# Kernel optimization log

Hardware: AMD Instinct MI355X
Metric: run time of the kernel (lower is better)

## Reference

```python
import jax, jax.numpy as jnp
import numpy as np

B, S, E = 32, 128, 128
NQ, NS = 100000, 512
QN, SN = 4, 10
S_MAX = 4
NEG = -1e30


def setup_inputs() -> dict:
    key = jax.random.key(0)
    ks = jax.random.split(key, 24)
    def nrm(k, shape, sc):
        return jax.random.normal(k, shape, jnp.float32) * sc
    inp = {}
    inp['question'] = jax.random.randint(ks[0], (B, S), 0, NQ, jnp.int32)
    inp['response'] = jax.random.randint(ks[1], (B, S), 0, 2, jnp.int32)
    inp['mask'] = jax.random.randint(ks[2], (B, S), 0, 2, jnp.int32)
    inp['q_neighbors'] = jax.random.randint(ks[3], (NQ, QN), 0, NS, jnp.int32)
    inp['s_neighbors'] = jax.random.randint(ks[4], (NS, SN), 0, NQ, jnp.int32)
    sidx = jax.random.randint(ks[5], (NQ, S_MAX), 0, NS, jnp.int32)
    inp['qs_table'] = jnp.zeros((NQ, NS), jnp.float32).at[jnp.arange(NQ)[:, None], sidx].set(1.0)
    inp['emb_q'] = nrm(ks[6], (NQ, E), 1.0)
    inp['emb_s'] = nrm(ks[7], (NS, E), 1.0)
    inp['emb_r'] = nrm(ks[8], (2, E), 1.0)
    s_in = 1.0 / np.sqrt(2 * E).astype(np.float32)
    s_e = 1.0 / np.sqrt(E).astype(np.float32)
    inp['W_ih'] = nrm(ks[9], (4 * E, 2 * E), s_in)
    inp['b_ih'] = nrm(ks[10], (4 * E,), s_in)
    inp['b_hh'] = nrm(ks[11], (4 * E,), s_in)
    inp['W_agg'] = nrm(ks[12], (3, E, E), s_e)
    inp['b_agg'] = nrm(ks[13], (3, E), s_e)
    inp['W_last'] = nrm(ks[14], (E, E), s_e)
    inp['b_last'] = nrm(ks[15], (E,), s_e)
    inp['W_query'] = nrm(ks[16], (E, E), s_e)
    inp['b_query'] = nrm(ks[17], (E,), s_e)
    inp['W_key'] = nrm(ks[18], (E, E), s_e)
    inp['b_key'] = nrm(ks[19], (E,), s_e)
    inp['w_W'] = nrm(ks[20], (2 * E,), s_in)
    inp['b_W'] = nrm(ks[21], (), s_in)
    return inp


def _forward(question, response, mask, q_neighbors, s_neighbors, qs_table,
             emb_q, emb_s, emb_r, W_ih, b_ih, b_hh, W_agg, b_agg, W_last, b_last,
             W_query, b_query, W_key, b_key, w_W, b_W):
    Bq, Sq = question.shape
    Ed = emb_q.shape[1]
    AGG = W_agg.shape[0]
    w_q, w_k = w_W[:Ed], w_W[Ed:]
    c_pad = jnp.tanh(b_query) @ w_k  # attention logit piece of an all-zero padded state
    pos = jnp.arange(Sq)

    def step(state_history, xs):
        t, q_t, r_t, m_t, q_next = xs
        # ---- multi-hop neighbor gather (q -> s -> q -> s) ----
        n1 = q_neighbors[q_t]              # [B,QN] skill ids
        n2 = s_neighbors[n1]               # [B,QN,SN] question ids
        n3 = q_neighbors[n2]               # [B,QN,SN,QN] skill ids
        e = [emb_q[q_t], emb_s[n1], emb_q[n2], emb_s[n3]]
        # triangular mean-aggregate (dropout is identity in eval mode)
        for i in range(AGG):
            for j in range(AGG - i):
                e[j] = jnp.tanh((e[j + 1].mean(-2) + e[j]) @ W_agg[j].T + b_agg[j])
        agg = jnp.tanh(e[0] @ W_last.T + b_last)
        emb_qt = jnp.where((m_t == 1)[:, None], agg, emb_q[q_t])
        # ---- LSTMCell with zero initial (h, c): W_hh @ 0 drops out, b_hh remains ----
        x = jnp.concatenate([emb_qt, emb_r[r_t]], -1)
        gates = x @ W_ih.T + b_ih + b_hh
        gi, gf, gg, go = jnp.split(gates, 4, -1)
        h = jax.nn.sigmoid(go) * jnp.tanh(jax.nn.sigmoid(gi) * jnp.tanh(gg))
        # ---- skills related to next question; zero-padded rows contribute exactly 0 ----
        vals, sidx = jax.lax.top_k(qs_table[q_next], S_MAX)
        emb_sk = emb_s[sidx] * (vals > 0.0)[..., None]
        qs_concat = jnp.concatenate([emb_q[q_next][:, None], emb_sk], 1)  # [B,1+S_MAX,E]
        # ---- hard recap: history steps whose question is a 2-hop neighbor of q_next ----
        q_rel = s_neighbors[q_neighbors[q_next]].reshape(Bq, -1)          # [B,QN*SN]
        matches = (question[:, :, None] == q_rel[:, None, :]).any(-1) & (pos[None, :] < t)
        n_sel = matches.sum(-1)
        P = (jnp.max(n_sel) - n_sel).astype(jnp.float32)  # zero-pad count to per-batch max
        # ---- predict: MLP_W(concat(Q,K)) is rank-1 => logit = a[b,q] + c[b,s] ----
        a = jnp.tanh(qs_concat @ W_key.T + b_key) @ w_q + b_W             # [B,Qd]
        c_hist = jnp.tanh(state_history @ W_query.T + b_query) @ w_k      # [B,S]
        c_cur = jnp.tanh(h @ W_query.T + b_query) @ w_k                   # [B]
        lh = jnp.where(matches[:, None, :], a[:, :, None] + c_hist[:, None, :], NEG)
        lc = a + c_cur[:, None]
        lp = a + c_pad
        m = jnp.maximum(jnp.maximum(lh.max(-1), lc), lp)
        Eh = jnp.exp(lh - m[:, :, None])
        Ec = jnp.exp(lc - m)
        Ep = jnp.exp(lp - m)
        g_hist = jnp.einsum('bqe,bse->bqs', qs_concat, state_history)
        g_cur = jnp.einsum('bqe,be->bq', qs_concat, h)
        denom = Eh.sum(-1) + Ec + P[:, None] * Ep  # zero-pad states counted analytically
        num = (Eh * g_hist).sum(-1) + Ec * g_cur   # pads multiply g=0 -> no numerator term
        y = jax.nn.sigmoid(jnp.sum(num / denom, axis=1))
        # original skips the state write at t == 0 (slot 0 stays zero forever)
        state_history = state_history.at[:, t].set(jnp.where(t > 0, h, jnp.zeros_like(h)))
        return state_history, y

    ts = jnp.arange(Sq - 1)
    xs = (ts, question[:, :-1].T, response[:, :-1].T, mask[:, :-1].T, question[:, 1:].T)
    init = jnp.zeros((Bq, Sq, Ed), jnp.float32)
    _, ys = jax.lax.scan(step, init, xs)
    return jnp.zeros((Bq, Sq), jnp.float32).at[:, 0].set(0.5).at[:, 1:].set(ys.T)


def reference(question, response, mask, q_neighbors, s_neighbors, qs_table,
              emb_q, emb_s, emb_r, W_ih, b_ih, b_hh, W_agg, b_agg, W_last, b_last,
              W_query, b_query, W_key, b_key, w_W, b_W):
    return _forward(question, response, mask, q_neighbors, s_neighbors, qs_table,
                    emb_q, emb_s, emb_r, W_ih, b_ih, b_hh, W_agg, b_agg, W_last, b_last,
                    W_query, b_query, W_key, b_key, w_W, b_W)
```

## Files before the change

kernel.cpp:

```cpp
#include <hip/hip_runtime.h>
#include <stdint.h>

#define NB 32
#define SEQ 128
#define EMB 128
#define NSTEP 127
#define NS 512

__device__ __forceinline__ float ftanh(float x){ float e=__expf(2.f*x); return 1.f-2.f/(e+1.f); }
__device__ __forceinline__ float fsig(float x){ return 1.f/(1.f+__expf(-x)); }
__device__ __forceinline__ float4 ld4(const float* p){ return *(const float4*)p; }

#define FMA4(acc, xv, a0, a1, a2, a3) \
  acc.x = fmaf(xv.x, a0.x, fmaf(xv.y, a1.x, fmaf(xv.z, a2.x, fmaf(xv.w, a3.x, acc.x)))); \
  acc.y = fmaf(xv.x, a0.y, fmaf(xv.y, a1.y, fmaf(xv.z, a2.y, fmaf(xv.w, a3.y, acc.y)))); \
  acc.z = fmaf(xv.x, a0.z, fmaf(xv.y, a1.z, fmaf(xv.z, a2.z, fmaf(xv.w, a3.z, acc.z)))); \
  acc.w = fmaf(xv.x, a0.w, fmaf(xv.y, a1.w, fmaf(xv.z, a2.w, fmaf(xv.w, a3.w, acc.w))));

template<int K, int XS>
__device__ __forceinline__ void gemm8(const float* __restrict__ WT, int NEtot,
                                      const float* __restrict__ Xl,
                                      const float* __restrict__ bias,
                                      float* __restrict__ outb )
{
  const int tid = threadIdx.x;
  const int et = tid & 31;
  const int rt = tid >> 5;
  const float* wp = WT + et*4;
  const float* xr = Xl + rt*XS;
  constexpr int G = K/4;
  float4 acc = {0.f,0.f,0.f,0.f};
  float4 w0 = ld4(wp);
  float4 w1 = ld4(wp + NEtot);
  float4 w2 = ld4(wp + 2*NEtot);
  float4 w3 = ld4(wp + 3*NEtot);
  const float* wq = wp + (size_t)4*NEtot;
  float4 m0 = ld4(wq);
  float4 m1 = ld4(wq + NEtot);
  float4 m2 = ld4(wq + 2*NEtot);
  float4 m3 = ld4(wq + 3*NEtot);
  #pragma unroll 2
  for (int g = 0; g + 2 < G; g += 2) {
    const float* wa = wp + (size_t)(4*(g+2))*NEtot;
    float4 n0 = ld4(wa);
    float4 n1 = ld4(wa + NEtot);
    float4 n2 = ld4(wa + 2*NEtot);
    float4 n3 = ld4(wa + 3*NEtot);
    float4 xa = ld4(xr + 4*g);
    FMA4(acc, xa, w0, w1, w2, w3);
    w0=n0; w1=n1; w2=n2; w3=n3;
    const float* wb = wp + (size_t)(4*(g+3))*NEtot;
    float4 o0 = ld4(wb);
    float4 o1 = ld4(wb + NEtot);
    float4 o2 = ld4(wb + 2*NEtot);
    float4 o3 = ld4(wb + 3*NEtot);
    float4 xb = ld4(xr + 4*(g+1));
    FMA4(acc, xb, m0, m1, m2, m3);
    m0=o0; m1=o1; m2=o2; m3=o3;
  }
  {
    float4 xa = ld4(xr + 4*(G-2));
    FMA4(acc, xa, w0, w1, w2, w3);
    float4 xb = ld4(xr + 4*(G-1));
    FMA4(acc, xb, m0, m1, m2, m3);
  }
  float4 bb = ld4(bias + et*4);
  acc.x+=bb.x; acc.y+=bb.y; acc.z+=bb.z; acc.w+=bb.w;
  *(float4*)(outb + rt*132 + et*4) = acc;
}

__global__ __launch_bounds__(256) void k_T(
    const float* __restrict__ W_agg, const float* __restrict__ W_last,
    const float* __restrict__ W_query, const float* __restrict__ W_ih,
    const float* __restrict__ b_ih, const float* __restrict__ b_hh,
    const float* __restrict__ b_query, const float* __restrict__ w_W,
    float* __restrict__ WT012, float* __restrict__ WLT, float* __restrict__ WQT,
    float* __restrict__ WIHT, float* __restrict__ BIH, float* __restrict__ CPAD,
    float* __restrict__ G1, int* __restrict__ Pmaxi)
{
  const int gid = blockIdx.x*256 + threadIdx.x;
  const int gsz = gridDim.x*256;
  for (int i = gid; i < 49152; i += gsz) {
    int j = i >> 14, rem = i & 16383, k = rem >> 7, e = rem & 127;
    WT012[i] = W_agg[j*16384 + e*128 + k];
  }
  for (int i = gid; i < 16384; i += gsz) {
    int k = i >> 7, e = i & 127;
    WLT[i] = W_last[e*128 + k];
    WQT[i] = W_query[e*128 + k];
  }
  for (int i = gid; i < 131072; i += gsz) {
    int k = i >> 9, e = i & 511;
    WIHT[i] = W_ih[e*256 + k];
  }
  for (int i = gid; i < 65536; i += gsz) G1[i] = 0.f;
  for (int i = gid; i < 512; i += gsz) BIH[i] = b_ih[i] + b_hh[i];
  for (int i = gid; i < 128; i += gsz) Pmaxi[i] = 0;
  if (blockIdx.x == 0) {
    __shared__ float red[256];
    float v = (threadIdx.x < 128) ? ftanh(b_query[threadIdx.x]) * w_W[128 + threadIdx.x] : 0.f;
    red[threadIdx.x] = v; __syncthreads();
    #pragma unroll
    for (int s = 128; s > 0; s >>= 1) {
      if (threadIdx.x < s) red[threadIdx.x] += red[threadIdx.x + s];
      __syncthreads();
    }
    if (threadIdx.x == 0) CPAD[0] = red[0];
  }
}

__global__ __launch_bounds__(256) void k_pre(
    const int* __restrict__ s_neighbors, const int* __restrict__ q_neighbors,
    const float* __restrict__ emb_q, const float* __restrict__ emb_s,
    const float* __restrict__ WT012, const float* __restrict__ b_agg,
    float* __restrict__ E1, float* __restrict__ G1)
{
  __shared__ float XA[8*132];
  __shared__ float XB[8*132];
  __shared__ int idx[80];
  __shared__ int n3[32];
  const int tid = threadIdx.x;
  const int blk = blockIdx.x;
  if (blk < 64) {
    const int s0 = blk*8;
    if (tid < 80) idx[tid] = s_neighbors[s0*10 + tid];
    __syncthreads();
    {
      int r = tid >> 5, e4 = (tid & 31) << 2;
      float4 a = ld4(emb_s + (size_t)(s0+r)*128 + e4);
      float sx=0,sy=0,sz=0,sw=0;
      #pragma unroll
      for (int jj = 0; jj < 10; ++jj) {
        float4 q = ld4(emb_q + (size_t)idx[r*10+jj]*128 + e4);
        sx+=q.x; sy+=q.y; sz+=q.z; sw+=q.w;
      }
      float4 o; o.x=a.x+0.1f*sx; o.y=a.y+0.1f*sy; o.z=a.z+0.1f*sz; o.w=a.w+0.1f*sw;
      *(float4*)(XA + r*132 + e4) = o;
    }
    __syncthreads();
    gemm8<128,132>(WT012 + 16384, 128, XA, b_agg + 128, XB);
    __syncthreads();
    for (int f = tid; f < 1024; f += 256) {
      int r = f >> 7, e = f & 127;
      E1[(size_t)(s0+r)*128 + e] = ftanh(XB[r*132 + e]);
    }
  } else {
    const int p0 = (blk-64)*8;
    if (tid < 8) idx[tid] = s_neighbors[p0 + tid];
    __syncthreads();
    if (tid < 32) n3[tid] = q_neighbors[(size_t)idx[tid>>2]*4 + (tid&3)];
    __syncthreads();
    {
      int r = tid >> 5, e4 = (tid & 31) << 2;
      float4 a = ld4(emb_q + (size_t)idx[r]*128 + e4);
      float sx=0,sy=0,sz=0,sw=0;
      #pragma unroll
      for (int k = 0; k < 4; ++k) {
        float4 q = ld4(emb_s + (size_t)n3[r*4+k]*128 + e4);
        sx+=q.x; sy+=q.y; sz+=q.z; sw+=q.w;
      }
      float4 o; o.x=a.x+0.25f*sx; o.y=a.y+0.25f*sy; o.z=a.z+0.25f*sz; o.w=a.w+0.25f*sw;
      *(float4*)(XA + r*132 + e4) = o;
    }
    __syncthreads();
    gemm8<128,132>(WT012 + 32768, 128, XA, b_agg + 256, XB);
    __syncthreads();
    for (int f = tid; f < 1024; f += 256) {
      int r = f >> 7, e = f & 127;
      atomicAdd(&G1[(size_t)((p0+r)/10)*128 + e], ftanh(XB[r*132 + e]));
    }
  }
}

__global__ __launch_bounds__(256) void k_pre2(
    const float* __restrict__ E1, const float* __restrict__ G1,
    const float* __restrict__ WT012, const float* __restrict__ b_agg,
    float* __restrict__ E2)
{
  __shared__ float XA[8*132];
  __shared__ float XB[8*132];
  const int tid = threadIdx.x;
  const int s0 = blockIdx.x*8;
  for (int f = tid; f < 1024; f += 256) {
    int r = f >> 7, e = f & 127;
    XA[r*132 + e] = 0.1f*G1[(size_t)(s0+r)*128 + e] + E1[(size_t)(s0+r)*128 + e];
  }
  __syncthreads();
  gemm8<128,132>(WT012 + 16384, 128, XA, b_agg + 128, XB);
  __syncthreads();
  for (int f = tid; f < 1024; f += 256) {
    int r = f >> 7, e = f & 127;
    E2[(size_t)(s0+r)*128 + e] = ftanh(XB[r*132 + e]);
  }
}

__global__ __launch_bounds__(256) void k_chain(
    const int* __restrict__ question, const int* __restrict__ response,
    const int* __restrict__ maskp, const int* __restrict__ q_neighbors,
    const float* __restrict__ emb_q, const float* __restrict__ emb_s,
    const float* __restrict__ emb_r,
    const float* __restrict__ WT012, const float* __restrict__ WLT,
    const float* __restrict__ WQT, const float* __restrict__ WIHT,
    const float* __restrict__ BIH,
    const float* __restrict__ b_agg, const float* __restrict__ b_last,
    const float* __restrict__ b_query, const float* __restrict__ w_W,
    const float* __restrict__ E1, const float* __restrict__ E2,
    float* __restrict__ Hfull, float* __restrict__ Cq)
{
  __shared__ float XA[8*132];
  __shared__ float XB[8*132];
  __shared__ float M1[8*132];
  __shared__ float M2[8*132];
  __shared__ float XC[8*264];
  __shared__ int qts[8], rts[8], mts[8], n1s[32];

  const int tid = threadIdx.x;
  const int blk = blockIdx.x;

  if (tid < 8) {
    int rid = blk*8 + tid;
    int b = rid / 127, t = rid - b*127;
    qts[tid] = question[b*SEQ + t];
    rts[tid] = response[b*SEQ + t];
    mts[tid] = maskp[b*SEQ + t];
  }
  __syncthreads();
  if (tid < 32) n1s[tid] = q_neighbors[(size_t)qts[tid>>2]*4 + (tid&3)];
  __syncthreads();
  {
    int r = tid >> 5, e4 = (tid & 31) << 2;
    const int* nn = n1s + r*4;
    float4 a = ld4(emb_q + (size_t)qts[r]*128 + e4);
    float s1x=0,s1y=0,s1z=0,s1w=0, s2x=0,s2y=0,s2z=0,s2w=0, s3x=0,s3y=0,s3z=0,s3w=0;
    #pragma unroll
    for (int i = 0; i < 4; ++i) {
      float4 q1 = ld4(emb_s + (size_t)nn[i]*128 + e4);
      float4 q2 = ld4(E1 + (size_t)nn[i]*128 + e4);
      float4 q3 = ld4(E2 + (size_t)nn[i]*128 + e4);
      s1x+=q1.x; s1y+=q1.y; s1z+=q1.z; s1w+=q1.w;
      s2x+=q2.x; s2y+=q2.y; s2z+=q2.z; s2w+=q2.w;
      s3x+=q3.x; s3y+=q3.y; s3z+=q3.z; s3w+=q3.w;
    }
    float4 o; o.x=a.x+0.25f*s1x; o.y=a.y+0.25f*s1y; o.z=a.z+0.25f*s1z; o.w=a.w+0.25f*s1w;
    *(float4*)(XA + r*132 + e4) = o;
    float4 p; p.x=0.25f*s2x; p.y=0.25f*s2y; p.z=0.25f*s2z; p.w=0.25f*s2w;
    *(float4*)(M1 + r*132 + e4) = p;
    float4 u; u.x=0.25f*s3x; u.y=0.25f*s3y; u.z=0.25f*s3z; u.w=0.25f*s3w;
    *(float4*)(M2 + r*132 + e4) = u;
  }
  __syncthreads();
  gemm8<128,132>(WT012, 128, XA, b_agg, XB);
  __syncthreads();
  for (int f = tid; f < 1056; f += 256) XB[f] = M1[f] + ftanh(XB[f]);
  __syncthreads();
  gemm8<128,132>(WT012, 128, XB, b_agg, XA);
  __syncthreads();
  for (int f = tid; f < 1056; f += 256) XA[f] = M2[f] + ftanh(XA[f]);
  __syncthreads();
  gemm8<128,132>(WT012, 128, XA, b_agg, XB);
  __syncthreads();
  for (int f = tid; f < 1056; f += 256) XB[f] = ftanh(XB[f]);
  __syncthreads();
  gemm8<128,132>(WLT, 128, XB, b_last, XA);
  __syncthreads();
  for (int f = tid; f < 1024; f += 256) {
    int r = f >> 7, e = f & 127;
    float agg = ftanh(XA[r*132 + e]);
    XC[r*264 + e] = (mts[r] == 1) ? agg : emb_q[(size_t)qts[r]*128 + e];
    XC[r*264 + 128 + e] = emb_r[rts[r]*128 + e];
  }
  __syncthreads();
  gemm8<256,264>(WIHT,       512, XC, BIH,       XA);
  gemm8<256,264>(WIHT + 256, 512, XC, BIH + 256, XB);
  gemm8<256,264>(WIHT + 384, 512, XC, BIH + 384, M1);
  __syncthreads();
  for (int f = tid; f < 1024; f += 256) {
    int r = f >> 7, e = f & 127;
    float gi = XA[r*132 + e], gg = XB[r*132 + e], go = M1[r*132 + e];
    float h = fsig(go) * ftanh(fsig(gi) * ftanh(gg));
    XC[r*264 + e] = h;
    Hfull[(size_t)(blk*8 + r)*128 + e] = h;
  }
  __syncthreads();
  gemm8<128,264>(WQT, 128, XC, b_query, XA);
  __syncthreads();
  {
    const int et = tid & 31, rt = tid >> 5;
    float4 o = ld4(XA + rt*132 + et*4);
    float4 wv = ld4(w_W + 128 + et*4);
    float s = ftanh(o.x)*wv.x + ftanh(o.y)*wv.y + ftanh(o.z)*wv.z + ftanh(o.w)*wv.w;
    #pragma unroll
    for (int off = 16; off > 0; off >>= 1) s += __shfl_down(s, off);
    if (et == 0) Cq[blk*8 + rt] = s;
  }
}

__global__ __launch_bounds__(64) void k_match(
    const int* __restrict__ question, const int* __restrict__ q_neighbors,
    const int* __restrict__ s_neighbors,
    int* __restrict__ nsel, unsigned long long* __restrict__ mwords,
    int* __restrict__ Pmaxi)
{
  __shared__ int qr[40];
  const int tid = threadIdx.x;
  const int t = blockIdx.x;
  const int b = blockIdx.y;
  const int q_next = question[b*SEQ + t + 1];
  if (tid < 40)
    qr[tid] = s_neighbors[(size_t)q_neighbors[(size_t)q_next*4 + tid/10]*10 + tid%10];
  __syncthreads();
  int q0 = question[b*SEQ + tid];
  int q1 = question[b*SEQ + 64 + tid];
  bool p0 = false, p1 = false;
  #pragma unroll 8
  for (int i = 0; i < 40; ++i) { p0 |= (q0 == qr[i]); p1 |= (q1 == qr[i]); }
  p0 &= (tid < t);
  p1 &= (64 + tid < t);
  unsigned long long w0 = __ballot(p0);
  unsigned long long w1 = __ballot(p1);
  if (tid == 0) {
    mwords[((size_t)b*NSTEP + t)*2 + 0] = w0;
    mwords[((size_t)b*NSTEP + t)*2 + 1] = w1;
    int ns = __popcll(w0) + __popcll(w1);
    nsel[b*NSTEP + t] = ns;
    atomicMax(&Pmaxi[t], ns);
  }
}

__device__ __forceinline__ float wredsum(float v) {
  #pragma unroll
  for (int o = 32; o > 0; o >>= 1) v += __shfl_down(v, o);
  return v;
}
__device__ __forceinline__ float wredmax(float v) {
  #pragma unroll
  for (int o = 32; o > 0; o >>= 1) v = fmaxf(v, __shfl_down(v, o));
  return v;
}

__global__ __launch_bounds__(128) void k_attn(
    const int* __restrict__ question, const float* __restrict__ qs_table,
    const float* __restrict__ emb_q, const float* __restrict__ emb_s,
    const float* __restrict__ CPAD,
    const float* __restrict__ Hfull, const float* __restrict__ Cq,
    const int* __restrict__ nsel, const unsigned long long* __restrict__ mwords,
    const int* __restrict__ Pmaxi, float* __restrict__ out)
{
  __shared__ float us[128];
  __shared__ int cols[8];
  __shared__ int cnt;
  __shared__ float smx[2];
  __shared__ float s3[2][3];
  const int tid = threadIdx.x;
  const int wid = tid >> 6;
  const int bid = blockIdx.x;
  const int b = bid / NSTEP, t = bid % NSTEP;
  const size_t bt = (size_t)b*NSTEP + t;
  const int q_next = question[b*SEQ + t + 1];

  if (tid == 0) cnt = 0;
  __syncthreads();
  {
    float4 v = ld4(qs_table + (size_t)q_next*NS + tid*4);
    if (v.x > 0.f) { int p = atomicAdd(&cnt, 1); if (p < 8) cols[p] = tid*4; }
    if (v.y > 0.f) { int p = atomicAdd(&cnt, 1); if (p < 8) cols[p] = tid*4+1; }
    if (v.z > 0.f) { int p = atomicAdd(&cnt, 1); if (p < 8) cols[p] = tid*4+2; }
    if (v.w > 0.f) { int p = atomicAdd(&cnt, 1); if (p < 8) cols[p] = tid*4+3; }
  }
  __syncthreads();
  const int nc = min(cnt, 4);
  {
    float ue = emb_q[(size_t)q_next*EMB + tid];
    for (int i = 0; i < nc; ++i) ue += emb_s[(size_t)cols[i]*EMB + tid];
    us[tid] = ue;
  }
  const float c_pad = CPAD[0];
  const float P = (float)(Pmaxi[t] - nsel[bt]);

  const unsigned long long w0 = mwords[bt*2 + 0];
  const unsigned long long w1 = mwords[bt*2 + 1];
  const bool matched = (tid < 64) ? ((w0 >> tid) & 1ull)
                                  : ((w1 >> (tid - 64)) & 1ull);
  const float c_cur = Cq[bt];
  float Cp = matched ? ((tid == 0) ? c_pad : Cq[(size_t)b*NSTEP + tid]) : -3.0e38f;
  float mh = wredmax(Cp);
  if ((tid & 63) == 0) smx[wid] = mh;
  __syncthreads();
  float M = fmaxf(fmaxf(smx[0], smx[1]), fmaxf(c_cur, c_pad));
  float wgt = matched ? __expf(Cp - M) : 0.f;
  float dotp = 0.f;
  if (matched && tid >= 1) {
    const float* hp = Hfull + ((size_t)b*NSTEP + tid)*EMB;
    float s = 0.f;
    #pragma unroll 8
    for (int e = 0; e < 128; e += 4) {
      float4 h4 = ld4(hp + e);
      s = fmaf(us[e],h4.x, fmaf(us[e+1],h4.y, fmaf(us[e+2],h4.z, fmaf(us[e+3],h4.w, s))));
    }
    dotp = s;
  }
  float gcp = us[tid] * Hfull[bt*EMB + tid];
  float a0 = wredsum(wgt);
  float a1 = wredsum(wgt * dotp);
  float a2 = wredsum(gcp);
  if ((tid & 63) == 0) { s3[wid][0] = a0; s3[wid][1] = a1; s3[wid][2] = a2; }
  __syncthreads();
  if (tid == 0) {
    float Sexp = s3[0][0] + s3[1][0];
    float Snum = s3[0][1] + s3[1][1];
    float gc   = s3[0][2] + s3[1][2];
    float Ec = __expf(c_cur - M), Ep = __expf(c_pad - M);
    float D = Sexp + Ec + P * Ep;
    float numt = Snum + Ec * gc;
    out[b*SEQ + t + 1] = fsig(numt / D);
    if (t == 0) out[b*SEQ] = 0.5f;
  }
}

extern "C" void kernel_launch(void* const* d_in, const int* in_sizes, int n_in,
                              void* d_out, int out_size, void* d_ws, size_t ws_size,
                              hipStream_t stream) {
  const int* question    = (const int*)d_in[0];
  const int* response    = (const int*)d_in[1];
  const int* maskp       = (const int*)d_in[2];
  const int* q_neighbors = (const int*)d_in[3];
  const int* s_neighbors = (const int*)d_in[4];
  const float* qs_table  = (const float*)d_in[5];
  const float* emb_q     = (const float*)d_in[6];
  const float* emb_s     = (const float*)d_in[7];
  const float* emb_r     = (const float*)d_in[8];
  const float* W_ih      = (const float*)d_in[9];
  const float* b_ih      = (const float*)d_in[10];
  const float* b_hh      = (const float*)d_in[11];
  const float* W_agg     = (const float*)d_in[12];
  const float* b_agg     = (const float*)d_in[13];
  const float* W_last    = (const float*)d_in[14];
  const float* b_last    = (const float*)d_in[15];
  const float* W_query   = (const float*)d_in[16];
  const float* b_query   = (const float*)d_in[17];
  const float* w_W       = (const float*)d_in[20];
  float* out = (float*)d_out;

  float* ws = (float*)d_ws;
  float* WT012 = ws;
  float* WLT   = ws + 49152;
  float* WQT   = ws + 65536;
  float* WIHT  = ws + 81920;
  float* BIH   = ws + 212992;
  float* CPAD  = ws + 213504;
  float* E1    = ws + 213520;
  float* G1    = ws + 279056;
  float* E2    = ws + 344592;
  float* Hfull = ws + 410128;
  float* Cq    = ws + 930320;
  int*   Pmaxi = (int*)(ws + 934384);
  int*   nselp = (int*)(ws + 934512);
  unsigned long long* mwords =
      (unsigned long long*)(((uintptr_t)(ws + 938576) + 15) & ~(uintptr_t)15);

  k_T<<<dim3(64), dim3(256), 0, stream>>>(
      W_agg, W_last, W_query, W_ih, b_ih, b_hh, b_query, w_W,
      WT012, WLT, WQT, WIHT, BIH, CPAD, G1, Pmaxi);
  k_pre<<<dim3(704), dim3(256), 0, stream>>>(
      s_neighbors, q_neighbors, emb_q, emb_s, WT012, b_agg, E1, G1);
  k_pre2<<<dim3(64), dim3(256), 0, stream>>>(E1, G1, WT012, b_agg, E2);
  k_chain<<<dim3(508), dim3(256), 0, stream>>>(
      question, response, maskp, q_neighbors, emb_q, emb_s, emb_r,
      WT012, WLT, WQT, WIHT, BIH, b_agg, b_last, b_query, w_W,
      E1, E2, Hfull, Cq);
  k_match<<<dim3(NSTEP, NB), dim3(64), 0, stream>>>(
      question, q_neighbors, s_neighbors, nselp, mwords, Pmaxi);
  k_attn<<<dim3(NB*NSTEP), dim3(128), 0, stream>>>(
      question, qs_table, emb_q, emb_s, CPAD, Hfull, Cq,
      nselp, mwords, Pmaxi, out);
}
```

Measured before the change: 430.1 us.

## Fuse all stages into one persistent kernel with grid-wide atomic barriers

Replaces the six separate launches (transpose, two precompute passes, chain, match, attention) with one persistent 512-block kernel that runs each stage in turn, separated by software grid barriers built on agent-scope atomics and a spin-wait. The match work is folded into the transpose phase and the attention work is batched two units per block. The aim is to remove per-launch overhead and inter-kernel idle gaps. In exchange it relies on all 512 blocks being co-resident (launch_bounds 256,2), otherwise the barriers deadlock, and it adds spin-wait and barrier latency between stages.

After: 701.0 us. +63.0%, slower.

```diff
diff --git a/kernel.cpp b/kernel.cpp
--- a/kernel.cpp
+++ b/kernel.cpp
@@ -6,6 +6,8 @@
 #define EMB 128
 #define NSTEP 127
 #define NS 512
+#define NBLK 512
+#define NUNIT 4064
 
 __device__ __forceinline__ float ftanh(float x){ float e=__expf(2.f*x); return 1.f-2.f/(e+1.f); }
 __device__ __forceinline__ float fsig(float x){ return 1.f/(1.f+__expf(-x)); }
@@ -19,9 +21,8 @@
 
 template<int K, int XS>
 __device__ __forceinline__ void gemm8(const float* __restrict__ WT, int NEtot,
-                                      const float* __restrict__ Xl,
-                                      const float* __restrict__ bias,
-                                      float* __restrict__ outb )
+                                      const float* Xl, const float* __restrict__ bias,
+                                      float* outb )
 {
   const int tid = threadIdx.x;
   const int et = tid & 31;
@@ -69,264 +70,6 @@
   *(float4*)(outb + rt*132 + et*4) = acc;
 }
 
-__global__ __launch_bounds__(256) void k_T(
-    const float* __restrict__ W_agg, const float* __restrict__ W_last,
-    const float* __restrict__ W_query, const float* __restrict__ W_ih,
-    const float* __restrict__ b_ih, const float* __restrict__ b_hh,
-    const float* __restrict__ b_query, const float* __restrict__ w_W,
-    float* __restrict__ WT012, float* __restrict__ WLT, float* __restrict__ WQT,
-    float* __restrict__ WIHT, float* __restrict__ BIH, float* __restrict__ CPAD,
-    float* __restrict__ G1, int* __restrict__ Pmaxi)
-{
-  const int gid = blockIdx.x*256 + threadIdx.x;
-  const int gsz = gridDim.x*256;
-  for (int i = gid; i < 49152; i += gsz) {
-    int j = i >> 14, rem = i & 16383, k = rem >> 7, e = rem & 127;
-    WT012[i] = W_agg[j*16384 + e*128 + k];
-  }
-  for (int i = gid; i < 16384; i += gsz) {
-    int k = i >> 7, e = i & 127;
-    WLT[i] = W_last[e*128 + k];
-    WQT[i] = W_query[e*128 + k];
-  }
-  for (int i = gid; i < 131072; i += gsz) {
-    int k = i >> 9, e = i & 511;
-    WIHT[i] = W_ih[e*256 + k];
-  }
-  for (int i = gid; i < 65536; i += gsz) G1[i] = 0.f;
-  for (int i = gid; i < 512; i += gsz) BIH[i] = b_ih[i] + b_hh[i];
-  for (int i = gid; i < 128; i += gsz) Pmaxi[i] = 0;
-  if (blockIdx.x == 0) {
-    __shared__ float red[256];
-    float v = (threadIdx.x < 128) ? ftanh(b_query[threadIdx.x]) * w_W[128 + threadIdx.x] : 0.f;
-    red[threadIdx.x] = v; __syncthreads();
-    #pragma unroll
-    for (int s = 128; s > 0; s >>= 1) {
-      if (threadIdx.x < s) red[threadIdx.x] += red[threadIdx.x + s];
-      __syncthreads();
-    }
-    if (threadIdx.x == 0) CPAD[0] = red[0];
-  }
-}
-
-__global__ __launch_bounds__(256) void k_pre(
-    const int* __restrict__ s_neighbors, const int* __restrict__ q_neighbors,
-    const float* __restrict__ emb_q, const float* __restrict__ emb_s,
-    const float* __restrict__ WT012, const float* __restrict__ b_agg,
-    float* __restrict__ E1, float* __restrict__ G1)
-{
-  __shared__ float XA[8*132];
-  __shared__ float XB[8*132];
-  __shared__ int idx[80];
-  __shared__ int n3[32];
-  const int tid = threadIdx.x;
-  const int blk = blockIdx.x;
-  if (blk < 64) {
-    const int s0 = blk*8;
-    if (tid < 80) idx[tid] = s_neighbors[s0*10 + tid];
-    __syncthreads();
-    {
-      int r = tid >> 5, e4 = (tid & 31) << 2;
-      float4 a = ld4(emb_s + (size_t)(s0+r)*128 + e4);
-      float sx=0,sy=0,sz=0,sw=0;
-      #pragma unroll
-      for (int jj = 0; jj < 10; ++jj) {
-        float4 q = ld4(emb_q + (size_t)idx[r*10+jj]*128 + e4);
-        sx+=q.x; sy+=q.y; sz+=q.z; sw+=q.w;
-      }
-      float4 o; o.x=a.x+0.1f*sx; o.y=a.y+0.1f*sy; o.z=a.z+0.1f*sz; o.w=a.w+0.1f*sw;
-      *(float4*)(XA + r*132 + e4) = o;
-    }
-    __syncthreads();
-    gemm8<128,132>(WT012 + 16384, 128, XA, b_agg + 128, XB);
-    __syncthreads();
-    for (int f = tid; f < 1024; f += 256) {
-      int r = f >> 7, e = f & 127;
-      E1[(size_t)(s0+r)*128 + e] = ftanh(XB[r*132 + e]);
-    }
-  } else {
-    const int p0 = (blk-64)*8;
-    if (tid < 8) idx[tid] = s_neighbors[p0 + tid];
-    __syncthreads();
-    if (tid < 32) n3[tid] = q_neighbors[(size_t)idx[tid>>2]*4 + (tid&3)];
-    __syncthreads();
-    {
-      int r = tid >> 5, e4 = (tid & 31) << 2;
-      float4 a = ld4(emb_q + (size_t)idx[r]*128 + e4);
-      float sx=0,sy=0,sz=0,sw=0;
-      #pragma unroll
-      for (int k = 0; k < 4; ++k) {
-        float4 q = ld4(emb_s + (size_t)n3[r*4+k]*128 + e4);
-        sx+=q.x; sy+=q.y; sz+=q.z; sw+=q.w;
-      }
-      float4 o; o.x=a.x+0.25f*sx; o.y=a.y+0.25f*sy; o.z=a.z+0.25f*sz; o.w=a.w+0.25f*sw;
-      *(float4*)(XA + r*132 + e4) = o;
-    }
-    __syncthreads();
-    gemm8<128,132>(WT012 + 32768, 128, XA, b_agg + 256, XB);
-    __syncthreads();
-    for (int f = tid; f < 1024; f += 256) {
-      int r = f >> 7, e = f & 127;
-      atomicAdd(&G1[(size_t)((p0+r)/10)*128 + e], ftanh(XB[r*132 + e]));
-    }
-  }
-}
-
-__global__ __launch_bounds__(256) void k_pre2(
-    const float* __restrict__ E1, const float* __restrict__ G1,
-    const float* __restrict__ WT012, const float* __restrict__ b_agg,
-    float* __restrict__ E2)
-{
-  __shared__ float XA[8*132];
-  __shared__ float XB[8*132];
-  const int tid = threadIdx.x;
-  const int s0 = blockIdx.x*8;
-  for (int f = tid; f < 1024; f += 256) {
-    int r = f >> 7, e = f & 127;
-    XA[r*132 + e] = 0.1f*G1[(size_t)(s0+r)*128 + e] + E1[(size_t)(s0+r)*128 + e];
-  }
-  __syncthreads();
-  gemm8<128,132>(WT012 + 16384, 128, XA, b_agg + 128, XB);
-  __syncthreads();
-  for (int f = tid; f < 1024; f += 256) {
-    int r = f >> 7, e = f & 127;
-    E2[(size_t)(s0+r)*128 + e] = ftanh(XB[r*132 + e]);
-  }
-}
-
-__global__ __launch_bounds__(256) void k_chain(
-    const int* __restrict__ question, const int* __restrict__ response,
-    const int* __restrict__ maskp, const int* __restrict__ q_neighbors,
-    const float* __restrict__ emb_q, const float* __restrict__ emb_s,
-    const float* __restrict__ emb_r,
-    const float* __restrict__ WT012, const float* __restrict__ WLT,
-    const float* __restrict__ WQT, const float* __restrict__ WIHT,
-    const float* __restrict__ BIH,
-    const float* __restrict__ b_agg, const float* __restrict__ b_last,
-    const float* __restrict__ b_query, const float* __restrict__ w_W,
-    const float* __restrict__ E1, const float* __restrict__ E2,
-    float* __restrict__ Hfull, float* __restrict__ Cq)
-{
-  __shared__ float XA[8*132];
-  __shared__ float XB[8*132];
-  __shared__ float M1[8*132];
-  __shared__ float M2[8*132];
-  __shared__ float XC[8*264];
-  __shared__ int qts[8], rts[8], mts[8], n1s[32];
-
-  const int tid = threadIdx.x;
-  const int blk = blockIdx.x;
-
-  if (tid < 8) {
-    int rid = blk*8 + tid;
-    int b = rid / 127, t = rid - b*127;
-    qts[tid] = question[b*SEQ + t];
-    rts[tid] = response[b*SEQ + t];
-    mts[tid] = maskp[b*SEQ + t];
-  }
-  __syncthreads();
-  if (tid < 32) n1s[tid] = q_neighbors[(size_t)qts[tid>>2]*4 + (tid&3)];
-  __syncthreads();
-  {
-    int r = tid >> 5, e4 = (tid & 31) << 2;
-    const int* nn = n1s + r*4;
-    float4 a = ld4(emb_q + (size_t)qts[r]*128 + e4);
-    float s1x=0,s1y=0,s1z=0,s1w=0, s2x=0,s2y=0,s2z=0,s2w=0, s3x=0,s3y=0,s3z=0,s3w=0;
-    #pragma unroll
-    for (int i = 0; i < 4; ++i) {
-      float4 q1 = ld4(emb_s + (size_t)nn[i]*128 + e4);
-      float4 q2 = ld4(E1 + (size_t)nn[i]*128 + e4);
-      float4 q3 = ld4(E2 + (size_t)nn[i]*128 + e4);
-      s1x+=q1.x; s1y+=q1.y; s1z+=q1.z; s1w+=q1.w;
-      s2x+=q2.x; s2y+=q2.y; s2z+=q2.z; s2w+=q2.w;
-      s3x+=q3.x; s3y+=q3.y; s3z+=q3.z; s3w+=q3.w;
-    }
-    float4 o; o.x=a.x+0.25f*s1x; o.y=a.y+0.25f*s1y; o.z=a.z+0.25f*s1z; o.w=a.w+0.25f*s1w;
-    *(float4*)(XA + r*132 + e4) = o;
-    float4 p; p.x=0.25f*s2x; p.y=0.25f*s2y; p.z=0.25f*s2z; p.w=0.25f*s2w;
-    *(float4*)(M1 + r*132 + e4) = p;
-    float4 u; u.x=0.25f*s3x; u.y=0.25f*s3y; u.z=0.25f*s3z; u.w=0.25f*s3w;
-    *(float4*)(M2 + r*132 + e4) = u;
-  }
-  __syncthreads();
-  gemm8<128,132>(WT012, 128, XA, b_agg, XB);
-  __syncthreads();
-  for (int f = tid; f < 1056; f += 256) XB[f] = M1[f] + ftanh(XB[f]);
-  __syncthreads();
-  gemm8<128,132>(WT012, 128, XB, b_agg, XA);
-  __syncthreads();
-  for (int f = tid; f < 1056; f += 256) XA[f] = M2[f] + ftanh(XA[f]);
-  __syncthreads();
-  gemm8<128,132>(WT012, 128, XA, b_agg, XB);
-  __syncthreads();
-  for (int f = tid; f < 1056; f += 256) XB[f] = ftanh(XB[f]);
-  __syncthreads();
-  gemm8<128,132>(WLT, 128, XB, b_last, XA);
-  __syncthreads();
-  for (int f = tid; f < 1024; f += 256) {
-    int r = f >> 7, e = f & 127;
-    float agg = ftanh(XA[r*132 + e]);
-    XC[r*264 + e] = (mts[r] == 1) ? agg : emb_q[(size_t)qts[r]*128 + e];
-    XC[r*264 + 128 + e] = emb_r[rts[r]*128 + e];
-  }
-  __syncthreads();
-  gemm8<256,264>(WIHT,       512, XC, BIH,       XA);
-  gemm8<256,264>(WIHT + 256, 512, XC, BIH + 256, XB);
-  gemm8<256,264>(WIHT + 384, 512, XC, BIH + 384, M1);
-  __syncthreads();
-  for (int f = tid; f < 1024; f += 256) {
-    int r = f >> 7, e = f & 127;
-    float gi = XA[r*132 + e], gg = XB[r*132 + e], go = M1[r*132 + e];
-    float h = fsig(go) * ftanh(fsig(gi) * ftanh(gg));
-    XC[r*264 + e] = h;
-    Hfull[(size_t)(blk*8 + r)*128 + e] = h;
-  }
-  __syncthreads();
-  gemm8<128,264>(WQT, 128, XC, b_query, XA);
-  __syncthreads();
-  {
-    const int et = tid & 31, rt = tid >> 5;
-    float4 o = ld4(XA + rt*132 + et*4);
-    float4 wv = ld4(w_W + 128 + et*4);
-    float s = ftanh(o.x)*wv.x + ftanh(o.y)*wv.y + ftanh(o.z)*wv.z + ftanh(o.w)*wv.w;
-    #pragma unroll
-    for (int off = 16; off > 0; off >>= 1) s += __shfl_down(s, off);
-    if (et == 0) Cq[blk*8 + rt] = s;
-  }
-}
-
-__global__ __launch_bounds__(64) void k_match(
-    const int* __restrict__ question, const int* __restrict__ q_neighbors,
-    const int* __restrict__ s_neighbors,
-    int* __restrict__ nsel, unsigned long long* __restrict__ mwords,
-    int* __restrict__ Pmaxi)
-{
-  __shared__ int qr[40];
-  const int tid = threadIdx.x;
-  const int t = blockIdx.x;
-  const int b = blockIdx.y;
-  const int q_next = question[b*SEQ + t + 1];
-  if (tid < 40)
-    qr[tid] = s_neighbors[(size_t)q_neighbors[(size_t)q_next*4 + tid/10]*10 + tid%10];
-  __syncthreads();
-  int q0 = question[b*SEQ + tid];
-  int q1 = question[b*SEQ + 64 + tid];
-  bool p0 = false, p1 = false;
-  #pragma unroll 8
-  for (int i = 0; i < 40; ++i) { p0 |= (q0 == qr[i]); p1 |= (q1 == qr[i]); }
-  p0 &= (tid < t);
-  p1 &= (64 + tid < t);
-  unsigned long long w0 = __ballot(p0);
-  unsigned long long w1 = __ballot(p1);
-  if (tid == 0) {
-    mwords[((size_t)b*NSTEP + t)*2 + 0] = w0;
-    mwords[((size_t)b*NSTEP + t)*2 + 1] = w1;
-    int ns = __popcll(w0) + __popcll(w1);
-    nsel[b*NSTEP + t] = ns;
-    atomicMax(&Pmaxi[t], ns);
-  }
-}
-
 __device__ __forceinline__ float wredsum(float v) {
   #pragma unroll
   for (int o = 32; o > 0; o >>= 1) v += __shfl_down(v, o);
@@ -338,82 +81,351 @@
   return v;
 }
 
-__global__ __launch_bounds__(128) void k_attn(
-    const int* __restrict__ question, const float* __restrict__ qs_table,
+__device__ __forceinline__ void gsync(int* bar, int idx, int nb) {
+  __syncthreads();
+  if (threadIdx.x == 0) {
+    __threadfence();
+    int prev = __hip_atomic_fetch_add(&bar[idx*32], 1, __ATOMIC_ACQ_REL,
+                                      __HIP_MEMORY_SCOPE_AGENT);
+    if (prev == nb - 1) {
+      __hip_atomic_store(&bar[idx*32 + 16], 1, __ATOMIC_RELEASE,
+                         __HIP_MEMORY_SCOPE_AGENT);
+    } else {
+      while (__hip_atomic_load(&bar[idx*32 + 16], __ATOMIC_ACQUIRE,
+                               __HIP_MEMORY_SCOPE_AGENT) == 0)
+        __builtin_amdgcn_s_sleep(8);
+    }
+    __threadfence();
+  }
+  __syncthreads();
+}
+
+__global__ void k_zero(int* __restrict__ bar, int* __restrict__ Pmaxi) {
+  int i = threadIdx.x;
+  if (i < 128) bar[i] = 0;
+  if (i < 128) Pmaxi[i] = 0;
+}
+
+__global__ __launch_bounds__(256, 2) void k_fused(
+    const int* __restrict__ question, const int* __restrict__ response,
+    const int* __restrict__ maskp, const int* __restrict__ q_neighbors,
+    const int* __restrict__ s_neighbors, const float* __restrict__ qs_table,
     const float* __restrict__ emb_q, const float* __restrict__ emb_s,
-    const float* __restrict__ CPAD,
-    const float* __restrict__ Hfull, const float* __restrict__ Cq,
-    const int* __restrict__ nsel, const unsigned long long* __restrict__ mwords,
-    const int* __restrict__ Pmaxi, float* __restrict__ out)
+    const float* __restrict__ emb_r,
+    const float* __restrict__ W_ih, const float* __restrict__ b_ih,
+    const float* __restrict__ b_hh, const float* __restrict__ W_agg,
+    const float* __restrict__ b_agg, const float* __restrict__ W_last,
+    const float* __restrict__ b_last, const float* __restrict__ W_query,
+    const float* __restrict__ b_query, const float* __restrict__ w_W,
+    float* __restrict__ WT012, float* __restrict__ WLT, float* __restrict__ WQT,
+    float* __restrict__ WIHT, float* __restrict__ BIH, float* __restrict__ CPAD,
+    float* __restrict__ E1, float* __restrict__ G1, float* __restrict__ E2,
+    float* __restrict__ Hfull, float* __restrict__ Cq,
+    int* __restrict__ Pmaxi, int* __restrict__ nsel,
+    unsigned long long* __restrict__ mwords, int* __restrict__ bar,
+    float* __restrict__ out)
 {
-  __shared__ float us[128];
-  __shared__ int cols[8];
-  __shared__ int cnt;
-  __shared__ float smx[2];
-  __shared__ float s3[2][3];
+  __shared__ float pool[6336];
+  __shared__ int ipool[256];
+  __shared__ unsigned long long wvw[4];
+  float* XA = pool;
+  float* XB = pool + 1056;
+  float* M1 = pool + 2112;
+  float* M2 = pool + 3168;
+  float* XC = pool + 4224;
+
   const int tid = threadIdx.x;
-  const int wid = tid >> 6;
-  const int bid = blockIdx.x;
-  const int b = bid / NSTEP, t = bid % NSTEP;
-  const size_t bt = (size_t)b*NSTEP + t;
-  const int q_next = question[b*SEQ + t + 1];
-
-  if (tid == 0) cnt = 0;
-  __syncthreads();
+  const int blk = blockIdx.x;
+
   {
-    float4 v = ld4(qs_table + (size_t)q_next*NS + tid*4);
-    if (v.x > 0.f) { int p = atomicAdd(&cnt, 1); if (p < 8) cols[p] = tid*4; }
-    if (v.y > 0.f) { int p = atomicAdd(&cnt, 1); if (p < 8) cols[p] = tid*4+1; }
-    if (v.z > 0.f) { int p = atomicAdd(&cnt, 1); if (p < 8) cols[p] = tid*4+2; }
-    if (v.w > 0.f) { int p = atomicAdd(&cnt, 1); if (p < 8) cols[p] = tid*4+3; }
-  }
-  __syncthreads();
-  const int nc = min(cnt, 4);
+    const int gid = blk*256 + tid;
+    const int gsz = NBLK*256;
+    for (int i = gid; i < 49152; i += gsz) {
+      int j = i >> 14, rem = i & 16383, k = rem >> 7, e = rem & 127;
+      WT012[i] = W_agg[j*16384 + e*128 + k];
+    }
+    for (int i = gid; i < 16384; i += gsz) {
+      int k = i >> 7, e = i & 127;
+      WLT[i] = W_last[e*128 + k];
+      WQT[i] = W_query[e*128 + k];
+    }
+    for (int i = gid; i < 131072; i += gsz) {
+      int k = i >> 9, e = i & 511;
+      WIHT[i] = W_ih[e*256 + k];
+    }
+    for (int i = gid; i < 65536; i += gsz) G1[i] = 0.f;
+    if (gid < 512) BIH[gid] = b_ih[gid] + b_hh[gid];
+    if (blk == 0) {
+      float v = (tid < 128) ? ftanh(b_query[tid]) * w_W[128 + tid] : 0.f;
+      pool[tid] = v; __syncthreads();
+      #pragma unroll
+      for (int s = 128; s > 0; s >>= 1) {
+        if (tid < s) pool[tid] += pool[tid + s];
+        __syncthreads();
+      }
+      if (tid == 0) CPAD[0] = pool[0];
+      __syncthreads();
+    }
+    const int half = tid >> 7, lt = tid & 127;
+    for (int it = 0; it < 4; ++it) {
+      int u = blk*8 + it*2 + half;
+      if (u >= NUNIT) u = NUNIT - 1;
+      int b = u / NSTEP, t = u - b*NSTEP;
+      const int q_next = question[b*SEQ + t + 1];
+      int* qr = ipool + half*40;
+      if (lt < 40)
+        qr[lt] = s_neighbors[(size_t)q_neighbors[(size_t)q_next*4 + lt/10]*10 + lt%10];
+      __syncthreads();
+      int qp = question[b*SEQ + lt];
+      bool p = false;
+      #pragma unroll 8
+      for (int i = 0; i < 40; ++i) p |= (qp == qr[i]);
+      p &= (lt < t);
+      unsigned long long bal = __ballot(p);
+      if ((tid & 63) == 0) {
+        mwords[((size_t)b*NSTEP + t)*2 + ((tid >> 6) & 1)] = bal;
+        wvw[tid >> 6] = bal;
+      }
+      __syncthreads();
+      if (lt == 0) {
+        unsigned long long a0 = wvw[half*2], a1 = wvw[half*2 + 1];
+        int ns = __popcll(a0) + __popcll(a1);
+        nsel[b*NSTEP + t] = ns;
+        atomicMax(&Pmaxi[t], ns);
+      }
+      __syncthreads();
+    }
+  }
+  gsync(bar, 0, NBLK);
+
+  for (int u = blk; u < 704; u += NBLK) {
+    int* idx = ipool;
+    int* n3i = ipool + 80;
+    if (u < 64) {
+      const int s0 = u*8;
+      if (tid < 80) idx[tid] = s_neighbors[s0*10 + tid];
+      __syncthreads();
+      {
+        int r = tid >> 5, e4 = (tid & 31) << 2;
+        float4 a = ld4(emb_s + (size_t)(s0+r)*128 + e4);
+        float sx=0,sy=0,sz=0,sw=0;
+        #pragma unroll
+        for (int jj = 0; jj < 10; ++jj) {
+          float4 q = ld4(emb_q + (size_t)idx[r*10+jj]*128 + e4);
+          sx+=q.x; sy+=q.y; sz+=q.z; sw+=q.w;
+        }
+        float4 o; o.x=a.x+0.1f*sx; o.y=a.y+0.1f*sy; o.z=a.z+0.1f*sz; o.w=a.w+0.1f*sw;
+        *(float4*)(XA + r*132 + e4) = o;
+      }
+      __syncthreads();
+      gemm8<128,132>(WT012 + 16384, 128, XA, b_agg + 128, XB);
+      __syncthreads();
+      for (int f = tid; f < 1024; f += 256) {
+        int r = f >> 7, e = f & 127;
+        E1[(size_t)(s0+r)*128 + e] = ftanh(XB[r*132 + e]);
+      }
+    } else {
+      const int p0 = (u-64)*8;
+      if (tid < 8) idx[tid] = s_neighbors[p0 + tid];
+      __syncthreads();
+      if (tid < 32) n3i[tid] = q_neighbors[(size_t)idx[tid>>2]*4 + (tid&3)];
+      __syncthreads();
+      {
+        int r = tid >> 5, e4 = (tid & 31) << 2;
+        float4 a = ld4(emb_q + (size_t)idx[r]*128 + e4);
+        float sx=0,sy=0,sz=0,sw=0;
+        #pragma unroll
+        for (int k = 0; k < 4; ++k) {
+          float4 q = ld4(emb_s + (size_t)n3i[r*4+k]*128 + e4);
+          sx+=q.x; sy+=q.y; sz+=q.z; sw+=q.w;
+        }
+        float4 o; o.x=a.x+0.25f*sx; o.y=a.y+0.25f*sy; o.z=a.z+0.25f*sz; o.w=a.w+0.25f*sw;
+        *(float4*)(XA + r*132 + e4) = o;
+      }
+      __syncthreads();
+      gemm8<128,132>(WT012 + 32768, 128, XA, b_agg + 256, XB);
+      __syncthreads();
+      for (int f = tid; f < 1024; f += 256) {
+        int r = f >> 7, e = f & 127;
+        atomicAdd(&G1[(size_t)((p0+r)/10)*128 + e], ftanh(XB[r*132 + e]));
+      }
+    }
+    __syncthreads();
+  }
+  gsync(bar, 1, NBLK);
+
+  if (blk < 64) {
+    const int s0 = blk*8;
+    for (int f = tid; f < 1024; f += 256) {
+      int r = f >> 7, e = f & 127;
+      XA[r*132 + e] = 0.1f*G1[(size_t)(s0+r)*128 + e] + E1[(size_t)(s0+r)*128 + e];
+    }
+    __syncthreads();
+    gemm8<128,132>(WT012 + 16384, 128, XA, b_agg + 128, XB);
+    __syncthreads();
+    for (int f = tid; f < 1024; f += 256) {
+      int r = f >> 7, e = f & 127;
+      E2[(size_t)(s0+r)*128 + e] = ftanh(XB[r*132 + e]);
+    }
+  }
+  gsync(bar, 2, NBLK);
+
+  if (blk < 508) {
+    int* qts = ipool;
+    int* rts = ipool + 8;
+    int* mts = ipool + 16;
+    int* n1s = ipool + 24;
+    if (tid < 8) {
+      int rid = blk*8 + tid;
+      int b = rid / 127, t = rid - b*127;
+      qts[tid] = question[b*SEQ + t];
+      rts[tid] = response[b*SEQ + t];
+      mts[tid] = maskp[b*SEQ + t];
+    }
+    __syncthreads();
+    if (tid < 32) n1s[tid] = q_neighbors[(size_t)qts[tid>>2]*4 + (tid&3)];
+    __syncthreads();
+    {
+      int r = tid >> 5, e4 = (tid & 31) << 2;
+      const int* nn = n1s + r*4;
+      float4 a = ld4(emb_q + (size_t)qts[r]*128 + e4);
+      float s1x=0,s1y=0,s1z=0,s1w=0, s2x=0,s2y=0,s2z=0,s2w=0, s3x=0,s3y=0,s3z=0,s3w=0;
+      #pragma unroll
+      for (int i = 0; i < 4; ++i) {
+        float4 q1 = ld4(emb_s + (size_t)nn[i]*128 + e4);
+        float4 q2 = ld4(E1 + (size_t)nn[i]*128 + e4);
+        float4 q3 = ld4(E2 + (size_t)nn[i]*128 + e4);
+        s1x+=q1.x; s1y+=q1.y; s1z+=q1.z; s1w+=q1.w;
+        s2x+=q2.x; s2y+=q2.y; s2z+=q2.z; s2w+=q2.w;
+        s3x+=q3.x; s3y+=q3.y; s3z+=q3.z; s3w+=q3.w;
+      }
+      float4 o; o.x=a.x+0.25f*s1x; o.y=a.y+0.25f*s1y; o.z=a.z+0.25f*s1z; o.w=a.w+0.25f*s1w;
+      *(float4*)(XA + r*132 + e4) = o;
+      float4 p; p.x=0.25f*s2x; p.y=0.25f*s2y; p.z=0.25f*s2z; p.w=0.25f*s2w;
+      *(float4*)(M1 + r*132 + e4) = p;
+      float4 u; u.x=0.25f*s3x; u.y=0.25f*s3y; u.z=0.25f*s3z; u.w=0.25f*s3w;
+      *(float4*)(M2 + r*132 + e4) = u;
+    }
+    __syncthreads();
+    gemm8<128,132>(WT012, 128, XA, b_agg, XB);
+    __syncthreads();
+    for (int f = tid; f < 1056; f += 256) XB[f] = M1[f] + ftanh(XB[f]);
+    __syncthreads();
+    gemm8<128,132>(WT012, 128, XB, b_agg, XA);
+    __syncthreads();
+    for (int f = tid; f < 1056; f += 256) XA[f] = M2[f] + ftanh(XA[f]);
+    __syncthreads();
+    gemm8<128,132>(WT012, 128, XA, b_agg, XB);
+    __syncthreads();
+    for (int f = tid; f < 1056; f += 256) XB[f] = ftanh(XB[f]);
+    __syncthreads();
+    gemm8<128,132>(WLT, 128, XB, b_last, XA);
+    __syncthreads();
+    for (int f = tid; f < 1024; f += 256) {
+      int r = f >> 7, e = f & 127;
+      float agg = ftanh(XA[r*132 + e]);
+      XC[r*264 + e] = (mts[r] == 1) ? agg : emb_q[(size_t)qts[r]*128 + e];
+      XC[r*264 + 128 + e] = emb_r[rts[r]*128 + e];
+    }
+    __syncthreads();
+    gemm8<256,264>(WIHT,       512, XC, BIH,       XA);
+    gemm8<256,264>(WIHT + 256, 512, XC, BIH + 256, XB);
+    gemm8<256,264>(WIHT + 384, 512, XC, BIH + 384, M1);
+    __syncthreads();
+    for (int f = tid; f < 1024; f += 256) {
+      int r = f >> 7, e = f & 127;
+      float gi = XA[r*132 + e], gg = XB[r*132 + e], go = M1[r*132 + e];
+      float h = fsig(go) * ftanh(fsig(gi) * ftanh(gg));
+      XC[r*264 + e] = h;
+      Hfull[(size_t)(blk*8 + r)*128 + e] = h;
+    }
+    __syncthreads();
+    gemm8<128,264>(WQT, 128, XC, b_query, XA);
+    __syncthreads();
+    {
+      const int et = tid & 31, rt = tid >> 5;
+      float4 o = ld4(XA + rt*132 + et*4);
+      float4 wv = ld4(w_W + 128 + et*4);
+      float s = ftanh(o.x)*wv.x + ftanh(o.y)*wv.y + ftanh(o.z)*wv.z + ftanh(o.w)*wv.w;
+      #pragma unroll
+      for (int off = 16; off > 0; off >>= 1) s += __shfl_down(s, off);
+      if (et == 0) Cq[blk*8 + rt] = s;
+    }
+  }
+  gsync(bar, 3, NBLK);
+
   {
-    float ue = emb_q[(size_t)q_next*EMB + tid];
-    for (int i = 0; i < nc; ++i) ue += emb_s[(size_t)cols[i]*EMB + tid];
-    us[tid] = ue;
-  }
-  const float c_pad = CPAD[0];
-  const float P = (float)(Pmaxi[t] - nsel[bt]);
-
-  const unsigned long long w0 = mwords[bt*2 + 0];
-  const unsigned long long w1 = mwords[bt*2 + 1];
-  const bool matched = (tid < 64) ? ((w0 >> tid) & 1ull)
-                                  : ((w1 >> (tid - 64)) & 1ull);
-  const float c_cur = Cq[bt];
-  float Cp = matched ? ((tid == 0) ? c_pad : Cq[(size_t)b*NSTEP + tid]) : -3.0e38f;
-  float mh = wredmax(Cp);
-  if ((tid & 63) == 0) smx[wid] = mh;
-  __syncthreads();
-  float M = fmaxf(fmaxf(smx[0], smx[1]), fmaxf(c_cur, c_pad));
-  float wgt = matched ? __expf(Cp - M) : 0.f;
-  float dotp = 0.f;
-  if (matched && tid >= 1) {
-    const float* hp = Hfull + ((size_t)b*NSTEP + tid)*EMB;
-    float s = 0.f;
-    #pragma unroll 8
-    for (int e = 0; e < 128; e += 4) {
-      float4 h4 = ld4(hp + e);
-      s = fmaf(us[e],h4.x, fmaf(us[e+1],h4.y, fmaf(us[e+2],h4.z, fmaf(us[e+3],h4.w, s))));
-    }
-    dotp = s;
-  }
-  float gcp = us[tid] * Hfull[bt*EMB + tid];
-  float a0 = wredsum(wgt);
-  float a1 = wredsum(wgt * dotp);
-  float a2 = wredsum(gcp);
-  if ((tid & 63) == 0) { s3[wid][0] = a0; s3[wid][1] = a1; s3[wid][2] = a2; }
-  __syncthreads();
-  if (tid == 0) {
-    float Sexp = s3[0][0] + s3[1][0];
-    float Snum = s3[0][1] + s3[1][1];
-    float gc   = s3[0][2] + s3[1][2];
-    float Ec = __expf(c_cur - M), Ep = __expf(c_pad - M);
-    float D = Sexp + Ec + P * Ep;
-    float numt = Snum + Ec * gc;
-    out[b*SEQ + t + 1] = fsig(numt / D);
-    if (t == 0) out[b*SEQ] = 0.5f;
+    const int half = tid >> 7, lt = tid & 127;
+    const int widh = (tid >> 6) & 1;
+    float* us = pool + half*128;
+    float* smx = pool + 256 + half*2;
+    float* s3 = pool + 260 + half*6;
+    int* cols = ipool + half*8;
+    int* cntp = ipool + 16 + half;
+    const float c_pad = CPAD[0];
+    for (int it = 0; it < 4; ++it) {
+      int u = blk*8 + it*2 + half;
+      if (u >= NUNIT) u = NUNIT - 1;
+      const int b = u / NSTEP, t = u - b*NSTEP;
+      const size_t bt = (size_t)b*NSTEP + t;
+      const int q_next = question[b*SEQ + t + 1];
+      if (lt == 0) *cntp = 0;
+      __syncthreads();
+      {
+        float4 v = ld4(qs_table + (size_t)q_next*NS + lt*4);
+        if (v.x > 0.f) { int p = atomicAdd(cntp, 1); if (p < 8) cols[p] = lt*4; }
+        if (v.y > 0.f) { int p = atomicAdd(cntp, 1); if (p < 8) cols[p] = lt*4+1; }
+        if (v.z > 0.f) { int p = atomicAdd(cntp, 1); if (p < 8) cols[p] = lt*4+2; }
+        if (v.w > 0.f) { int p = atomicAdd(cntp, 1); if (p < 8) cols[p] = lt*4+3; }
+      }
+      __syncthreads();
+      const int nc = min(*cntp, 4);
+      {
+        float ue = emb_q[(size_t)q_next*EMB + lt];
+        for (int i = 0; i < nc; ++i) ue += emb_s[(size_t)cols[i]*EMB + lt];
+        us[lt] = ue;
+      }
+      const float P = (float)(Pmaxi[t] - nsel[bt]);
+      const unsigned long long w0 = mwords[bt*2 + 0];
+      const unsigned long long w1 = mwords[bt*2 + 1];
+      const bool matched = (lt < 64) ? ((w0 >> lt) & 1ull)
+                                     : ((w1 >> (lt - 64)) & 1ull);
+      const float c_cur = Cq[bt];
+      float Cp = matched ? ((lt == 0) ? c_pad : Cq[(size_t)b*NSTEP + lt]) : -3.0e38f;
+      float mh = wredmax(Cp);
+      if ((tid & 63) == 0) smx[widh] = mh;
+      __syncthreads();
+      float M = fmaxf(fmaxf(smx[0], smx[1]), fmaxf(c_cur, c_pad));
+      float wgt = matched ? __expf(Cp - M) : 0.f;
+      float dotp = 0.f;
+      if (matched && lt >= 1) {
+        const float* hp = Hfull + ((size_t)b*NSTEP + lt)*EMB;
+        float s = 0.f;
+        #pragma unroll 8
+        for (int e = 0; e < 128; e += 4) {
+          float4 h4 = ld4(hp + e);
+          s = fmaf(us[e],h4.x, fmaf(us[e+1],h4.y, fmaf(us[e+2],h4.z, fmaf(us[e+3],h4.w, s))));
+        }
+        dotp = s;
+      }
+      float gcp = us[lt] * Hfull[bt*EMB + lt];
+      float a0 = wredsum(wgt);
+      float a1 = wredsum(wgt * dotp);
+      float a2 = wredsum(gcp);
+      if ((tid & 63) == 0) { s3[widh*3+0] = a0; s3[widh*3+1] = a1; s3[widh*3+2] = a2; }
+      __syncthreads();
+      if (lt == 0) {
+        float Sexp = s3[0] + s3[3];
+        float Snum = s3[1] + s3[4];
+        float gc   = s3[2] + s3[5];
+        float Ec = __expf(c_cur - M), Ep = __expf(c_pad - M);
+        float D = Sexp + Ec + P * Ep;
+        float numt = Snum + Ec * gc;
+        out[b*SEQ + t + 1] = fsig(numt / D);
+        if (t == 0) out[b*SEQ] = 0.5f;
+      }
+      __syncthreads();
+    }
   }
 }
 
@@ -457,20 +469,13 @@
   int*   nselp = (int*)(ws + 934512);
   unsigned long long* mwords =
       (unsigned long long*)(((uintptr_t)(ws + 938576) + 15) & ~(uintptr_t)15);
-
-  k_T<<<dim3(64), dim3(256), 0, stream>>>(
-      W_agg, W_last, W_query, W_ih, b_ih, b_hh, b_query, w_W,
-      WT012, WLT, WQT, WIHT, BIH, CPAD, G1, Pmaxi);
-  k_pre<<<dim3(704), dim3(256), 0, stream>>>(
-      s_neighbors, q_neighbors, emb_q, emb_s, WT012, b_agg, E1, G1);
-  k_pre2<<<dim3(64), dim3(256), 0, stream>>>(E1, G1, WT012, b_agg, E2);
-  k_chain<<<dim3(508), dim3(256), 0, stream>>>(
-      question, response, maskp, q_neighbors, emb_q, emb_s, emb_r,
-      WT012, WLT, WQT, WIHT, BIH, b_agg, b_last, b_query, w_W,
-      E1, E2, Hfull, Cq);
-  k_match<<<dim3(NSTEP, NB), dim3(64), 0, stream>>>(
-      question, q_neighbors, s_neighbors, nselp, mwords, Pmaxi);
-  k_attn<<<dim3(NB*NSTEP), dim3(128), 0, stream>>>(
-      question, qs_table, emb_q, emb_s, CPAD, Hfull, Cq,
-      nselp, mwords, Pmaxi, out);
-}
+  int*   bar   = (int*)(ws + 955000);
+
+  k_zero<<<dim3(1), dim3(256), 0, stream>>>(bar, Pmaxi);
+  k_fused<<<dim3(NBLK), dim3(256), 0, stream>>>(
+      question, response, maskp, q_neighbors, s_neighbors, qs_table,
+      emb_q, emb_s, emb_r, W_ih, b_ih, b_hh, W_agg, b_agg, W_last, b_last,
+      W_query, b_query, w_W,
+      WT012, WLT, WQT, WIHT, BIH, CPAD, E1, G1, E2, Hfull, Cq,
+      Pmaxi, nselp, mwords, bar, out);
+}
```
